# Kernel optimization log

Measured on AMD Instinct MI355X. Metric: run time of the kernel, lower is better.

Reference implementation:

```python
import jax, jax.numpy as jnp
import numpy as np

B, T, D_MODEL = 4, 4096, 1024
H = 16
DH = D_MODEL // H
EPS = 1e-6
CHUNK = 128


def _feature(x):
    # elu(x) + 1
    return jnp.where(x > 0, x + 1.0, jnp.exp(x))


def _causal_dot_product(Q, K, V):
    """Q,K,V: [B,H,T,D]. out[t] = Q[t] @ sum_{s<=t} K[s]^T V[s]. Chunked scan, O(T*D^2)."""
    b, h, t, d = Q.shape
    nc = t // CHUNK
    mask = jnp.tril(jnp.ones((CHUNK, CHUNK), dtype=Q.dtype))
    # [NC, B, H, C, D]
    qs = jnp.moveaxis(Q.reshape(b, h, nc, CHUNK, d), 2, 0)
    ks = jnp.moveaxis(K.reshape(b, h, nc, CHUNK, d), 2, 0)
    vs = jnp.moveaxis(V.reshape(b, h, nc, CHUNK, d), 2, 0)

    def step(S, qkv):
        q, k, v = qkv  # each [B,H,C,D]
        attn = jnp.einsum('bhid,bhjd->bhij', q, k) * mask  # intra-chunk causal
        out = jnp.einsum('bhij,bhjd->bhid', attn, v) + jnp.einsum('bhid,bhde->bhie', q, S)
        S = S + jnp.einsum('bhcd,bhce->bhde', k, v)
        return S, out

    S0 = jnp.zeros((b, h, d, d), dtype=Q.dtype)
    _, outs = jax.lax.scan(step, S0, (qs, ks, vs))
    return jnp.moveaxis(outs, 0, 2).reshape(b, h, t, d)


def setup_inputs() -> dict:
    key = jax.random.key(0)
    ks = jax.random.split(key, 6)
    s = 0.02
    x = jax.random.normal(ks[0], (B, T, D_MODEL), dtype=jnp.float32)
    Wq = jax.random.normal(ks[1], (D_MODEL, D_MODEL), dtype=jnp.float32) * s
    Wk = jax.random.normal(ks[2], (D_MODEL, D_MODEL), dtype=jnp.float32) * s
    Wv = jax.random.normal(ks[3], (D_MODEL, D_MODEL), dtype=jnp.float32) * s
    Wo = jax.random.normal(ks[4], (D_MODEL, D_MODEL), dtype=jnp.float32) * s
    bo = jax.random.normal(ks[5], (D_MODEL,), dtype=jnp.float32) * s
    return {"x": x, "Wq": Wq, "Wk": Wk, "Wv": Wv, "Wo": Wo, "bo": bo}


def reference(x, Wq, Wk, Wv, Wo, bo):
    b, t, _ = x.shape
    def proj(W):
        return (x @ W).reshape(b, t, H, DH).transpose(0, 2, 1, 3)  # [B,H,T,Dh]
    Q = _feature(proj(Wq))
    K = _feature(proj(Wk))
    V = proj(Wv)
    # Faithful to source: cumsum over axis 1 of the [B,H,T,D] layout (head axis)
    Z = 1.0 / (jnp.einsum('bhtd,bhtd->bht', Q, jnp.cumsum(K, axis=1)) + EPS)
    unnorm = _causal_dot_product(Q, K, V)
    out = unnorm * Z[..., None]  # [B,H,T,Dh]
    out = out.transpose(0, 2, 1, 3).reshape(b, t, H * DH)
    return out @ Wo + bo  # dropout is identity in eval
```

## Files before the change

kernel.cpp:

```cpp
#include <hip/hip_runtime.h>
#include <hip/hip_bf16.h>

#define BATCH 4
#define SEQ   4096
#define DMODEL 1024
#define NH    16
#define DH    64
#define NCHUNK 32
#define CHUNKSZ 128
#define FEPS  1e-6f

typedef unsigned short ushort_t;
typedef __attribute__((ext_vector_type(8))) short short8;
typedef __attribute__((ext_vector_type(4))) float f32x4;

__device__ __forceinline__ float bf2f(ushort_t u) {
    union { unsigned int i; float f; } x; x.i = ((unsigned int)u) << 16; return x.f;
}
__device__ __forceinline__ ushort_t f2bf(float f) {
    union { float f; unsigned int i; } x; x.f = f;
    unsigned int lsb = (x.i >> 16) & 1u;
    x.i += 0x7fffu + lsb;
    return (ushort_t)(x.i >> 16);
}

__device__ __forceinline__ void load_lds16(const void* g, void* l) {
    __builtin_amdgcn_global_load_lds(
        (const __attribute__((address_space(1))) int*)g,
        (__attribute__((address_space(3))) int*)l, 16, 0, 0);
}

__global__ __launch_bounds__(256) void cvt_k(const float* __restrict__ X,
                                             ushort_t* __restrict__ Xb, int n4)
{
    int i = blockIdx.x * blockDim.x + threadIdx.x;
    int stride = gridDim.x * blockDim.x;
    for (; i < n4; i += stride) {
        float4 v = ((const float4*)X)[i];
        ushort4 u;
        u.x = f2bf(v.x); u.y = f2bf(v.y); u.z = f2bf(v.z); u.w = f2bf(v.w);
        ((ushort4*)Xb)[i] = u;
    }
}

__global__ __launch_bounds__(256) void wt_k(const float* __restrict__ W,
                                            ushort_t* __restrict__ WT)
{
    __shared__ float tile[32][33];
    int tx = threadIdx.x & 31, ty = threadIdx.x >> 5;
    int kb = blockIdx.x << 5, nb = blockIdx.y << 5;
#pragma unroll
    for (int i = 0; i < 4; i++)
        tile[ty + i * 8][tx] = W[(size_t)(kb + ty + i * 8) * DMODEL + nb + tx];
    __syncthreads();
#pragma unroll
    for (int i = 0; i < 4; i++)
        WT[(size_t)(nb + ty + i * 8) * DMODEL + kb + tx] = f2bf(tile[tx][ty + i * 8]);
}

#define TBM 256
#define TBN 256
#define TBK 32

template<int MODE>
__global__ __launch_bounds__(512, 2) void mgemm3_k(const ushort_t* __restrict__ Ap,
                                                   const ushort_t* __restrict__ Bt,
                                                   const float* __restrict__ bias,
                                                   void* __restrict__ Cp,
                                                   int M, int N, int K)
{
    __shared__ short smem[49152];
    const int tid = threadIdx.x;
    const int l  = tid & 63;
    const int w  = tid >> 6;
    const int wm = w >> 2, wn = w & 3;
    const int lr = l & 15;
    const int kc = l >> 4;

    const size_t m0 = (size_t)blockIdx.x * TBM;
    const size_t n0 = (size_t)blockIdx.y * TBN;

    f32x4 acc[8][4];
#pragma unroll
    for (int i = 0; i < 8; i++)
#pragma unroll
        for (int j = 0; j < 4; j++) acc[i][j] = (f32x4){0.f, 0.f, 0.f, 0.f};

    auto STAGE_PAIR = [&](int slot, int k0, int i) {
        short* Asl = smem + slot * 16384;
        short* Bsl = Asl + 8192;
        const int sa  = w * 2 + i;
        const int kch = sa >> 2;
        const int rb  = sa & 3;
        const int ldso = (kch * 256 + rb * 64) * 8;
        load_lds16(Ap + (m0 + rb * 64 + l) * (size_t)K + k0 + kch * 8, Asl + ldso);
        load_lds16(Bt + (n0 + rb * 64 + l) * (size_t)K + k0 + kch * 8, Bsl + ldso);
    };

    const int nt = K / TBK;
    STAGE_PAIR(0, 0, 0);   STAGE_PAIR(0, 0, 1);
    STAGE_PAIR(1, TBK, 0); STAGE_PAIR(1, TBK, 1);
    asm volatile("s_waitcnt vmcnt(4)" ::: "memory");
    __builtin_amdgcn_sched_barrier(0);
    __builtin_amdgcn_s_barrier();

    for (int t = 0; t < nt; ++t) {
        const short* Asl = smem + (t % 3) * 16384;
        const short* Bsl = Asl + 8192;
        const bool pre = (t + 2 < nt);
        const int pslot = (t + 2) % 3;
        const int pk0 = (t + 2) * TBK;

        if (pre) STAGE_PAIR(pslot, pk0, 0);
        short8 bf[4], af0[4];
#pragma unroll
        for (int nn = 0; nn < 4; nn++)
            bf[nn] = *(const short8*)(Bsl + (kc * 256 + wn * 64 + nn * 16 + lr) * 8);
#pragma unroll
        for (int mt = 0; mt < 4; mt++)
            af0[mt] = *(const short8*)(Asl + (kc * 256 + wm * 128 + mt * 16 + lr) * 8);
        __builtin_amdgcn_s_setprio(1);
#pragma unroll
        for (int mt = 0; mt < 4; mt++)
#pragma unroll
            for (int nn = 0; nn < 4; nn++)
                acc[mt][nn] = __builtin_amdgcn_mfma_f32_16x16x32_bf16(
                    af0[mt], bf[nn], acc[mt][nn], 0, 0, 0);
        __builtin_amdgcn_s_setprio(0);

        if (pre) STAGE_PAIR(pslot, pk0, 1);
        short8 af1[4];
#pragma unroll
        for (int mt = 0; mt < 4; mt++)
            af1[mt] = *(const short8*)(Asl + (kc * 256 + wm * 128 + (4 + mt) * 16 + lr) * 8);
        __builtin_amdgcn_s_setprio(1);
#pragma unroll
        for (int mt = 0; mt < 4; mt++)
#pragma unroll
            for (int nn = 0; nn < 4; nn++)
                acc[4 + mt][nn] = __builtin_amdgcn_mfma_f32_16x16x32_bf16(
                    af1[mt], bf[nn], acc[4 + mt][nn], 0, 0, 0);
        __builtin_amdgcn_s_setprio(0);

        if (pre) {
            asm volatile("s_waitcnt vmcnt(4)" ::: "memory");
        } else {
            asm volatile("s_waitcnt vmcnt(0)" ::: "memory");
        }
        asm volatile("s_waitcnt lgkmcnt(0)" ::: "memory");
        __builtin_amdgcn_sched_barrier(0);
        __builtin_amdgcn_s_barrier();
    }

#pragma unroll
    for (int mt = 0; mt < 8; mt++) {
#pragma unroll
        for (int nn = 0; nn < 4; nn++) {
#pragma unroll
            for (int j = 0; j < 4; j++) {
                int m = (int)m0 + wm * 128 + mt * 16 + (l >> 4) * 4 + j;
                int n = (int)n0 + wn * 64 + nn * 16 + lr;
                float v = acc[mt][nn][j];
                if (MODE == 2) {
                    ((float*)Cp)[(size_t)m * N + n] = v + bias[n];
                } else {
                    if (n < 2048) v = (v > 0.f) ? (v + 1.f) : __expf(v);
                    int tns = n >> 10, nnn = n & 1023;
                    int b_ = m >> 12, t_ = m & 4095, h_ = nnn >> 6, d_ = nnn & 63;
                    ushort_t* base = (ushort_t*)Cp + (size_t)tns * BATCH * SEQ * DMODEL;
                    base[((((size_t)b_ * NH + h_) * SEQ + t_) << 6) + d_] = f2bf(v);
                }
            }
        }
    }
}

__global__ __launch_bounds__(64) void z_k(const ushort_t* __restrict__ Q,
                                          const ushort_t* __restrict__ K,
                                          float* __restrict__ Z)
{
    int bt = blockIdx.x;
    int b_ = bt >> 12, t_ = bt & 4095;
    int d = threadIdx.x;
    float qv[NH], kv[NH];
    size_t base = (((size_t)b_ * NH) * SEQ + t_) * DH + d;
#pragma unroll
    for (int h = 0; h < NH; h++) {
        qv[h] = bf2f(Q[base + (size_t)h * SEQ * DH]);
        kv[h] = bf2f(K[base + (size_t)h * SEQ * DH]);
    }
    float ck = 0.f;
#pragma unroll
    for (int h = 0; h < NH; h++) {
        ck += kv[h];
        float p = qv[h] * ck;
#pragma unroll
        for (int off = 1; off < 64; off <<= 1) p += __shfl_xor(p, off, 64);
        if (d == 0) Z[((size_t)b_ * NH + h) * SEQ + t_] = 1.f / (p + FEPS);
    }
}

__global__ __launch_bounds__(256) void kv_k(const ushort_t* __restrict__ Kf,
                                            const ushort_t* __restrict__ Vf,
                                            float* __restrict__ Sloc)
{
    __shared__ short KTs[8192];
    __shared__ short VTs[8192];
    const int tid = threadIdx.x;
    const int l = tid & 63, w = tid >> 6;
    const int lr = l & 15, hi = l >> 4;
    const int blk = blockIdx.x;
    const size_t rowbase = ((size_t)(blk >> 5) * SEQ + (size_t)(blk & 31) * CHUNKSZ) * DH;
    const uint4* K16 = (const uint4*)(Kf + rowbase);
    const uint4* V16 = (const uint4*)(Vf + rowbase);
#pragma unroll
    for (int i = 0; i < 4; i++) {
        int idx = tid + i * 256;
        union { uint4 q; ushort_t us[8]; } kk, vv;
        kk.q = K16[idx]; vv.q = V16[idx];
        int j = idx >> 3, e0 = (idx & 7) << 3;
#pragma unroll
        for (int s = 0; s < 8; s++) {
            int off = ((j >> 3) * 64 + e0 + s) * 8 + (j & 7);
            KTs[off] = (short)kk.us[s];
            VTs[off] = (short)vv.us[s];
        }
    }
    __syncthreads();
    f32x4 acc[4];
#pragma unroll
    for (int nt = 0; nt < 4; nt++) acc[nt] = (f32x4){0.f, 0.f, 0.f, 0.f};
#pragma unroll
    for (int ks = 0; ks < 4; ks++) {
        short8 af = *(const short8*)(KTs + ((ks * 4 + hi) * 64 + w * 16 + lr) * 8);
        short8 bf[4];
#pragma unroll
        for (int nt = 0; nt < 4; nt++)
            bf[nt] = *(const short8*)(VTs + ((ks * 4 + hi) * 64 + nt * 16 + lr) * 8);
#pragma unroll
        for (int nt = 0; nt < 4; nt++)
            acc[nt] = __builtin_amdgcn_mfma_f32_16x16x32_bf16(af, bf[nt], acc[nt], 0, 0, 0);
    }
    float* outp = Sloc + (size_t)blk * DH * DH;
#pragma unroll
    for (int nt = 0; nt < 4; nt++)
#pragma unroll
        for (int jr = 0; jr < 4; jr++) {
            int d_ = w * 16 + hi * 4 + jr;
            int e_ = nt * 16 + lr;
            outp[d_ * DH + e_] = acc[nt][jr];
        }
}

__global__ __launch_bounds__(256) void scan_k(float* __restrict__ Sloc)
{
    int bh = blockIdx.x, seg = blockIdx.y;
    int e = seg * 256 + threadIdx.x;
    float* base = Sloc + (size_t)bh * NCHUNK * DH * DH + e;
    float acc = 0.f;
    float cur = base[0];
    for (int cc = 0; cc < NCHUNK; cc++) {
        float nxt = (cc + 1 < NCHUNK) ? base[(size_t)(cc + 1) * DH * DH] : 0.f;
        base[(size_t)cc * DH * DH] = acc;
        acc += cur;
        cur = nxt;
    }
}

__global__ __launch_bounds__(256) void attn_k(const ushort_t* __restrict__ Qf,
                                              const ushort_t* __restrict__ Kf,
                                              const ushort_t* __restrict__ Vf,
                                              const float* __restrict__ Sloc,
                                              const float* __restrict__ Z,
                                              ushort_t* __restrict__ A)
{
    __shared__ short smem[36864];
    short* Qs  = smem;
    short* Ks  = smem + 8192;
    short* Ps  = smem + 8192;
    short* VTs = smem + 24576;
    short* STs = smem + 32768;

    const int tid = threadIdx.x;
    const int l = tid & 63, w = tid >> 6;
    const int lr = l & 15, hi = l >> 4;
    const int blk = blockIdx.x;
    const int c = blk & (NCHUNK - 1), bh = blk >> 5;
    const int b_ = bh >> 4, h_ = bh & 15;
    const size_t rowbase = ((size_t)bh * SEQ + (size_t)c * CHUNKSZ) * DH;

#pragma unroll
    for (int ii = 0; ii < 4; ii++) {
        int s = w * 4 + ii;
        int kc2 = s >> 1, rh = (s & 1) << 6;
        int ldso = (kc2 * 128 + rh) * 8;
        load_lds16(Qf + rowbase + (size_t)(rh + l) * DH + kc2 * 8, Qs + ldso);
        load_lds16(Kf + rowbase + (size_t)(rh + l) * DH + kc2 * 8, Ks + ldso);
    }
    {
        const uint4* V16 = (const uint4*)(Vf + rowbase);
#pragma unroll
        for (int i = 0; i < 4; i++) {
            int idx = tid + i * 256;
            union { uint4 q; ushort_t us[8]; } vv;
            vv.q = V16[idx];
            int j = idx >> 3, e0 = (idx & 7) << 3;
#pragma unroll
            for (int s = 0; s < 8; s++)
                VTs[((j >> 3) * 64 + e0 + s) * 8 + (j & 7)] = (short)vv.us[s];
        }
    }
    {
        const float4* S16 = (const float4*)(Sloc + (size_t)blk * DH * DH);
#pragma unroll
        for (int i = 0; i < 4; i++) {
            int idx = tid + i * 256;
            float4 f = S16[idx];
            int d = idx >> 4, e0 = (idx & 15) << 2;
            STs[((d >> 3) * 64 + e0 + 0) * 8 + (d & 7)] = (short)f2bf(f.x);
            STs[((d >> 3) * 64 + e0 + 1) * 8 + (d & 7)] = (short)f2bf(f.y);
            STs[((d >> 3) * 64 + e0 + 2) * 8 + (d & 7)] = (short)f2bf(f.z);
            STs[((d >> 3) * 64 + e0 + 3) * 8 + (d & 7)] = (short)f2bf(f.w);
        }
    }
    __syncthreads();

    f32x4 acc1[2][8];
#pragma unroll
    for (int mt = 0; mt < 2; mt++)
#pragma unroll
        for (int nt = 0; nt < 8; nt++) acc1[mt][nt] = (f32x4){0.f, 0.f, 0.f, 0.f};
#pragma unroll
    for (int ks = 0; ks < 2; ks++) {
        short8 af[2], bf[8];
#pragma unroll
        for (int mt = 0; mt < 2; mt++)
            af[mt] = *(const short8*)(Qs + ((ks * 4 + hi) * 128 + w * 32 + mt * 16 + lr) * 8);
#pragma unroll
        for (int nt = 0; nt < 8; nt++)
            bf[nt] = *(const short8*)(Ks + ((ks * 4 + hi) * 128 + nt * 16 + lr) * 8);
#pragma unroll
        for (int mt = 0; mt < 2; mt++)
#pragma unroll
            for (int nt = 0; nt < 8; nt++)
                acc1[mt][nt] = __builtin_amdgcn_mfma_f32_16x16x32_bf16(
                    af[mt], bf[nt], acc1[mt][nt], 0, 0, 0);
    }
    __syncthreads();

#pragma unroll
    for (int mt = 0; mt < 2; mt++)
#pragma unroll
        for (int nt = 0; nt < 8; nt++)
#pragma unroll
            for (int jr = 0; jr < 4; jr++) {
                int i_ = w * 32 + mt * 16 + hi * 4 + jr;
                int j_ = nt * 16 + lr;
                float v = (j_ <= i_) ? acc1[mt][nt][jr] : 0.f;
                Ps[((j_ >> 3) * 128 + i_) * 8 + (j_ & 7)] = (short)f2bf(v);
            }
    __syncthreads();

    f32x4 acc2[2][4];
#pragma unroll
    for (int mt = 0; mt < 2; mt++)
#pragma unroll
        for (int nt = 0; nt < 4; nt++) acc2[mt][nt] = (f32x4){0.f, 0.f, 0.f, 0.f};
#pragma unroll
    for (int ks = 0; ks < 4; ks++) {
        short8 af[2], bf[4];
#pragma unroll
        for (int mt = 0; mt < 2; mt++)
            af[mt] = *(const short8*)(Ps + ((ks * 4 + hi) * 128 + w * 32 + mt * 16 + lr) * 8);
#pragma unroll
        for (int nt = 0; nt < 4; nt++)
            bf[nt] = *(const short8*)(VTs + ((ks * 4 + hi) * 64 + nt * 16 + lr) * 8);
#pragma unroll
        for (int mt = 0; mt < 2; mt++)
#pragma unroll
            for (int nt = 0; nt < 4; nt++)
                acc2[mt][nt] = __builtin_amdgcn_mfma_f32_16x16x32_bf16(
                    af[mt], bf[nt], acc2[mt][nt], 0, 0, 0);
    }
#pragma unroll
    for (int ks = 0; ks < 2; ks++) {
        short8 af[2], bf[4];
#pragma unroll
        for (int mt = 0; mt < 2; mt++)
            af[mt] = *(const short8*)(Qs + ((ks * 4 + hi) * 128 + w * 32 + mt * 16 + lr) * 8);
#pragma unroll
        for (int nt = 0; nt < 4; nt++)
            bf[nt] = *(const short8*)(STs + ((ks * 4 + hi) * 64 + nt * 16 + lr) * 8);
#pragma unroll
        for (int mt = 0; mt < 2; mt++)
#pragma unroll
            for (int nt = 0; nt < 4; nt++)
                acc2[mt][nt] = __builtin_amdgcn_mfma_f32_16x16x32_bf16(
                    af[mt], bf[nt], acc2[mt][nt], 0, 0, 0);
    }

#pragma unroll
    for (int mt = 0; mt < 2; mt++) {
#pragma unroll
        for (int jr = 0; jr < 4; jr++) {
            int i_ = w * 32 + mt * 16 + hi * 4 + jr;
            int t_ = c * CHUNKSZ + i_;
            float z = Z[(size_t)bh * SEQ + t_];
            ushort_t* op = A + (((size_t)(b_ * SEQ + t_)) * NH + h_) * DH;
#pragma unroll
            for (int nt = 0; nt < 4; nt++)
                op[nt * 16 + lr] = f2bf(acc2[mt][nt][jr] * z);
        }
    }
}

extern "C" void kernel_launch(void* const* d_in, const int* in_sizes, int n_in,
                              void* d_out, int out_size, void* d_ws, size_t ws_size,
                              hipStream_t stream)
{
    const float* x  = (const float*)d_in[0];
    const float* Wq = (const float*)d_in[1];
    const float* Wk = (const float*)d_in[2];
    const float* Wv = (const float*)d_in[3];
    const float* Wo = (const float*)d_in[4];
    const float* bo = (const float*)d_in[5];
    float* out = (float*)d_out;

    const size_t NEL = (size_t)BATCH * SEQ * DMODEL;
    const size_t WEL = (size_t)DMODEL * DMODEL;
    ushort_t* Qb  = (ushort_t*)d_ws;
    ushort_t* Kb  = Qb + NEL;
    ushort_t* Vb  = Kb + NEL;
    ushort_t* XAb = Vb + NEL;
    float*    Zb  = (float*)(XAb + NEL);
    ushort_t* WTq = (ushort_t*)(Zb + (size_t)BATCH * NH * SEQ);
    ushort_t* WTk = WTq + WEL;
    ushort_t* WTv = WTk + WEL;
    ushort_t* WTo = WTv + WEL;
    float*    Sl  = (float*)d_out;

    const int M = BATCH * SEQ;
    dim3 gw(32, 32);

    cvt_k<<<dim3(2048), dim3(256), 0, stream>>>(x, XAb, (int)(NEL / 4));
    wt_k<<<gw, dim3(256), 0, stream>>>(Wq, WTq);
    wt_k<<<gw, dim3(256), 0, stream>>>(Wk, WTk);
    wt_k<<<gw, dim3(256), 0, stream>>>(Wv, WTv);
    wt_k<<<gw, dim3(256), 0, stream>>>(Wo, WTo);

    mgemm3_k<0><<<dim3(M / TBM, 3 * DMODEL / TBN), dim3(512), 0, stream>>>(
        XAb, WTq, nullptr, Qb, M, 3 * DMODEL, DMODEL);

    z_k<<<dim3(BATCH * SEQ), dim3(64), 0, stream>>>(Qb, Kb, Zb);

    kv_k<<<dim3(BATCH * NH * NCHUNK), dim3(256), 0, stream>>>(Kb, Vb, Sl);
    scan_k<<<dim3(BATCH * NH, 16), dim3(256), 0, stream>>>(Sl);
    attn_k<<<dim3(BATCH * NH * NCHUNK), dim3(256), 0, stream>>>(Qb, Kb, Vb, Sl, Zb, XAb);

    mgemm3_k<2><<<dim3(M / TBM, DMODEL / TBN), dim3(512), 0, stream>>>(
        XAb, WTo, bo, out, M, DMODEL, DMODEL);
}
```

Baseline: 304.9 us.

## Deepen GEMM LDS pipeline to four stages, merge weight transposes, batch z_k rows

The GEMM kernel moves from a three-slot to a four-slot LDS ring, prefetching three K-tiles ahead, and adds mid-iteration barriers around the fragment loads so slot reuse stays safe. The four weight-transpose launches become one launch indexed by blockIdx.z, and z_k now packs four timesteps per 256-thread block. The aim is more hidden global-load latency and fewer small launches, at the cost of 128KB of LDS per block, which may limit occupancy to one block per CU, plus extra barriers per iteration.

New measurement: 293.9 us. 3.6% less time.

```diff
diff --git a/kernel.cpp b/kernel.cpp
--- a/kernel.cpp
+++ b/kernel.cpp
@@ -43,9 +43,15 @@
     }
 }
 
-__global__ __launch_bounds__(256) void wt_k(const float* __restrict__ W,
-                                            ushort_t* __restrict__ WT)
-{
+__global__ __launch_bounds__(256) void wt4_k(const float* __restrict__ W0,
+                                             const float* __restrict__ W1,
+                                             const float* __restrict__ W2,
+                                             const float* __restrict__ W3,
+                                             ushort_t* __restrict__ WT0)
+{
+    const float* Ws[4] = {W0, W1, W2, W3};
+    const float* W = Ws[blockIdx.z];
+    ushort_t* WT = WT0 + (size_t)blockIdx.z * DMODEL * DMODEL;
     __shared__ float tile[32][33];
     int tx = threadIdx.x & 31, ty = threadIdx.x >> 5;
     int kb = blockIdx.x << 5, nb = blockIdx.y << 5;
@@ -63,13 +69,13 @@
 #define TBK 32
 
 template<int MODE>
-__global__ __launch_bounds__(512, 2) void mgemm3_k(const ushort_t* __restrict__ Ap,
+__global__ __launch_bounds__(512, 2) void mgemm8_k(const ushort_t* __restrict__ Ap,
                                                    const ushort_t* __restrict__ Bt,
                                                    const float* __restrict__ bias,
                                                    void* __restrict__ Cp,
                                                    int M, int N, int K)
 {
-    __shared__ short smem[49152];
+    __shared__ short smem[65536];
     const int tid = threadIdx.x;
     const int l  = tid & 63;
     const int w  = tid >> 6;
@@ -98,18 +104,19 @@
     };
 
     const int nt = K / TBK;
-    STAGE_PAIR(0, 0, 0);   STAGE_PAIR(0, 0, 1);
-    STAGE_PAIR(1, TBK, 0); STAGE_PAIR(1, TBK, 1);
-    asm volatile("s_waitcnt vmcnt(4)" ::: "memory");
+    STAGE_PAIR(0, 0, 0);       STAGE_PAIR(0, 0, 1);
+    STAGE_PAIR(1, TBK, 0);     STAGE_PAIR(1, TBK, 1);
+    STAGE_PAIR(2, 2 * TBK, 0); STAGE_PAIR(2, 2 * TBK, 1);
+    asm volatile("s_waitcnt vmcnt(8)" ::: "memory");
     __builtin_amdgcn_sched_barrier(0);
     __builtin_amdgcn_s_barrier();
 
     for (int t = 0; t < nt; ++t) {
-        const short* Asl = smem + (t % 3) * 16384;
+        const short* Asl = smem + (t & 3) * 16384;
         const short* Bsl = Asl + 8192;
-        const bool pre = (t + 2 < nt);
-        const int pslot = (t + 2) % 3;
-        const int pk0 = (t + 2) * TBK;
+        const bool pre = (t + 3 < nt);
+        const int pslot = (t + 3) & 3;
+        const int pk0 = (t + 3) * TBK;
 
         if (pre) STAGE_PAIR(pslot, pk0, 0);
         short8 bf[4], af0[4];
@@ -119,6 +126,10 @@
 #pragma unroll
         for (int mt = 0; mt < 4; mt++)
             af0[mt] = *(const short8*)(Asl + (kc * 256 + wm * 128 + mt * 16 + lr) * 8);
+        __builtin_amdgcn_sched_barrier(0);
+        __builtin_amdgcn_s_barrier();
+        asm volatile("s_waitcnt lgkmcnt(0)" ::: "memory");
+        __builtin_amdgcn_sched_barrier(0);
         __builtin_amdgcn_s_setprio(1);
 #pragma unroll
         for (int mt = 0; mt < 4; mt++)
@@ -127,12 +138,17 @@
                 acc[mt][nn] = __builtin_amdgcn_mfma_f32_16x16x32_bf16(
                     af0[mt], bf[nn], acc[mt][nn], 0, 0, 0);
         __builtin_amdgcn_s_setprio(0);
+        __builtin_amdgcn_s_barrier();
 
         if (pre) STAGE_PAIR(pslot, pk0, 1);
         short8 af1[4];
 #pragma unroll
         for (int mt = 0; mt < 4; mt++)
             af1[mt] = *(const short8*)(Asl + (kc * 256 + wm * 128 + (4 + mt) * 16 + lr) * 8);
+        __builtin_amdgcn_sched_barrier(0);
+        __builtin_amdgcn_s_barrier();
+        asm volatile("s_waitcnt lgkmcnt(0)" ::: "memory");
+        __builtin_amdgcn_sched_barrier(0);
         __builtin_amdgcn_s_setprio(1);
 #pragma unroll
         for (int mt = 0; mt < 4; mt++)
@@ -142,12 +158,13 @@
                     af1[mt], bf[nn], acc[4 + mt][nn], 0, 0, 0);
         __builtin_amdgcn_s_setprio(0);
 
-        if (pre) {
+        if (t + 3 < nt) {
+            asm volatile("s_waitcnt vmcnt(8)" ::: "memory");
+        } else if (t + 2 < nt) {
             asm volatile("s_waitcnt vmcnt(4)" ::: "memory");
-        } else {
+        } else if (t + 1 < nt) {
             asm volatile("s_waitcnt vmcnt(0)" ::: "memory");
         }
-        asm volatile("s_waitcnt lgkmcnt(0)" ::: "memory");
         __builtin_amdgcn_sched_barrier(0);
         __builtin_amdgcn_s_barrier();
     }
@@ -175,13 +192,13 @@
     }
 }
 
-__global__ __launch_bounds__(64) void z_k(const ushort_t* __restrict__ Q,
-                                          const ushort_t* __restrict__ K,
-                                          float* __restrict__ Z)
-{
-    int bt = blockIdx.x;
+__global__ __launch_bounds__(256) void z_k(const ushort_t* __restrict__ Q,
+                                           const ushort_t* __restrict__ K,
+                                           float* __restrict__ Z)
+{
+    int bt = blockIdx.x * 4 + (threadIdx.x >> 6);
     int b_ = bt >> 12, t_ = bt & 4095;
-    int d = threadIdx.x;
+    int d = threadIdx.x & 63;
     float qv[NH], kv[NH];
     size_t base = (((size_t)b_ * NH) * SEQ + t_) * DH + d;
 #pragma unroll
@@ -434,29 +451,23 @@
     ushort_t* XAb = Vb + NEL;
     float*    Zb  = (float*)(XAb + NEL);
     ushort_t* WTq = (ushort_t*)(Zb + (size_t)BATCH * NH * SEQ);
-    ushort_t* WTk = WTq + WEL;
-    ushort_t* WTv = WTk + WEL;
-    ushort_t* WTo = WTv + WEL;
+    ushort_t* WTo = WTq + 3 * WEL;
     float*    Sl  = (float*)d_out;
 
     const int M = BATCH * SEQ;
-    dim3 gw(32, 32);
 
     cvt_k<<<dim3(2048), dim3(256), 0, stream>>>(x, XAb, (int)(NEL / 4));
-    wt_k<<<gw, dim3(256), 0, stream>>>(Wq, WTq);
-    wt_k<<<gw, dim3(256), 0, stream>>>(Wk, WTk);
-    wt_k<<<gw, dim3(256), 0, stream>>>(Wv, WTv);
-    wt_k<<<gw, dim3(256), 0, stream>>>(Wo, WTo);
-
-    mgemm3_k<0><<<dim3(M / TBM, 3 * DMODEL / TBN), dim3(512), 0, stream>>>(
+    wt4_k<<<dim3(32, 32, 4), dim3(256), 0, stream>>>(Wq, Wk, Wv, Wo, WTq);
+
+    mgemm8_k<0><<<dim3(M / TBM, 3 * DMODEL / TBN), dim3(512), 0, stream>>>(
         XAb, WTq, nullptr, Qb, M, 3 * DMODEL, DMODEL);
 
-    z_k<<<dim3(BATCH * SEQ), dim3(64), 0, stream>>>(Qb, Kb, Zb);
+    z_k<<<dim3(BATCH * SEQ / 4), dim3(256), 0, stream>>>(Qb, Kb, Zb);
 
     kv_k<<<dim3(BATCH * NH * NCHUNK), dim3(256), 0, stream>>>(Kb, Vb, Sl);
     scan_k<<<dim3(BATCH * NH, 16), dim3(256), 0, stream>>>(Sl);
     attn_k<<<dim3(BATCH * NH * NCHUNK), dim3(256), 0, stream>>>(Qb, Kb, Vb, Sl, Zb, XAb);
 
-    mgemm3_k<2><<<dim3(M / TBM, DMODEL / TBN), dim3(512), 0, stream>>>(
+    mgemm8_k<2><<<dim3(M / TBM, DMODEL / TBN), dim3(512), 0, stream>>>(
         XAb, WTo, bo, out, M, DMODEL, DMODEL);
 }
```
